# Optimization experiments

Measured on AMD Instinct MI355X. Metric: run time of the kernel, lower is better.

Reference implementation:

```python
import jax, jax.numpy as jnp
import numpy as np

N = 8192
E = 262144
IN_F = 128
OUT_F = 128


def setup_inputs() -> dict:
    key = jax.random.key(0)
    k1, k2, k3, k4 = jax.random.split(key, 4)
    x = jax.random.normal(k1, (N, IN_F), dtype=jnp.float32)
    adj = jax.random.randint(k2, (2, E), 0, N, dtype=jnp.int64)
    edge_w = jax.random.uniform(k3, (E,), dtype=jnp.float32)
    # Kaiming-normal-style init for weight (std = sqrt(2/fan_in)); zero bias.
    weight = jax.random.normal(k4, (IN_F, OUT_F), dtype=jnp.float32) * np.sqrt(2.0 / IN_F)
    bias = jnp.zeros((OUT_F,), dtype=jnp.float32)
    return {"x": x, "adj": adj, "edge_w": edge_w, "weight": weight, "bias": bias}


def reference(x, adj, edge_w, weight, bias):
    eps = 1e-10
    n = x.shape[0]
    support = x @ weight  # [N, out_features]
    # Densify COO adjacency (duplicate indices sum, matching sparse_coo_tensor.to_dense)
    adj_dense = jnp.zeros((n, n), dtype=x.dtype).at[adj[0], adj[1]].add(edge_w)
    adj_dense = adj_dense + jnp.eye(n, dtype=x.dtype)  # add self-loops
    deg = jnp.sum(adj_dense, axis=1)  # [N]
    d_inv_sqrt = 1.0 / jnp.sqrt(deg + eps)
    # D^{-1/2} A D^{-1/2} expressed as row/col scaling (same math as diag matmuls)
    norm_adj = d_inv_sqrt[:, None] * adj_dense * d_inv_sqrt[None, :]
    # include_bias=True path
    return norm_adj @ support + bias
```

## Files before the change

kernel.cpp:

```cpp
#include <hip/hip_runtime.h>
#include <math.h>

#define N_NODES 8192
#define NE      262144
#define F       128
#define CAP     96
#define NBLK    64
#define EPB     4096
#define GBLKS   256

#define FMA4(acc, xs, wq) \
    acc.x += (xs) * (wq).x; acc.y += (xs) * (wq).y; acc.z += (xs) * (wq).z; acc.w += (xs) * (wq).w;

__global__ __launch_bounds__(256) void k_fused(const float* __restrict__ x,
                                               const int* __restrict__ adj,
                                               const float* __restrict__ ew,
                                               const float* __restrict__ wmat,
                                               int* __restrict__ start_out,
                                               int2* __restrict__ bins,
                                               float* __restrict__ support) {
    __shared__ union {
        struct { int cnt[N_NODES]; int2 bin[EPB]; int part[256]; } e;
        struct { float xT[128][68]; float wl[128][68]; } g;
    } sh;
    int tid = threadIdx.x;

    if (blockIdx.x < NBLK) {
        int blk = blockIdx.x;
#pragma unroll
        for (int j = 0; j < 8; j++)
            *(int4*)&sh.e.cnt[tid * 4 + j * 1024] = make_int4(0, 0, 0, 0);
        __syncthreads();

        int base_e = blk * EPB + tid * 16;
        int4 r4[4];
#pragma unroll
        for (int ch = 0; ch < 4; ch++) r4[ch] = *(const int4*)(adj + base_e + ch * 4);
#pragma unroll
        for (int ch = 0; ch < 4; ch++) {
            atomicAdd(&sh.e.cnt[r4[ch].x], 1);
            atomicAdd(&sh.e.cnt[r4[ch].y], 1);
            atomicAdd(&sh.e.cnt[r4[ch].z], 1);
            atomicAdd(&sh.e.cnt[r4[ch].w], 1);
        }
        __syncthreads();

        int loc[32];
        int run = 0;
#pragma unroll
        for (int k = 0; k < 32; k++) { loc[k] = run; run += sh.e.cnt[tid * 32 + k]; }
        sh.e.part[tid] = run;
        __syncthreads();
        for (int off = 1; off < 256; off <<= 1) {
            int v = (tid >= off) ? sh.e.part[tid - off] : 0;
            __syncthreads();
            sh.e.part[tid] += v;
            __syncthreads();
        }
        int base0 = sh.e.part[tid] - run;
        __syncthreads();
#pragma unroll
        for (int k = 0; k < 32; k++) sh.e.cnt[tid * 32 + k] = base0 + loc[k];
        __syncthreads();
#pragma unroll
        for (int j = 0; j < 8; j++)
            *(int4*)&start_out[(size_t)blk * N_NODES + tid * 4 + j * 1024] =
                *(int4*)&sh.e.cnt[tid * 4 + j * 1024];
        __syncthreads();

#pragma unroll
        for (int ch = 0; ch < 4; ch++) {
            int e0 = base_e + ch * 4;
            int4   cc = *(const int4*)(adj + NE + e0);
            float4 wv = *(const float4*)(ew + e0);
            int pos;
            pos = atomicAdd(&sh.e.cnt[r4[ch].x], 1); sh.e.bin[pos] = make_int2(cc.x, __float_as_int(wv.x));
            pos = atomicAdd(&sh.e.cnt[r4[ch].y], 1); sh.e.bin[pos] = make_int2(cc.y, __float_as_int(wv.y));
            pos = atomicAdd(&sh.e.cnt[r4[ch].z], 1); sh.e.bin[pos] = make_int2(cc.z, __float_as_int(wv.z));
            pos = atomicAdd(&sh.e.cnt[r4[ch].w], 1); sh.e.bin[pos] = make_int2(cc.w, __float_as_int(wv.w));
        }
        __syncthreads();
#pragma unroll
        for (int j = 0; j < 8; j++)
            ((int4*)bins)[(size_t)blk * 2048 + tid + j * 256] =
                ((int4*)sh.e.bin)[tid + j * 256];
        return;
    }

    int g   = blockIdx.x - NBLK;
    int R0  = (g >> 1) * 64;
    int chf = g & 1;
    {
        int row = tid & 63;
        int w0  = tid >> 6;
        const float* xr = x + (size_t)(R0 + row) * F;
#pragma unroll
        for (int j = 0; j < 8; j++) {
            int c0 = w0 * 4 + 16 * j;
            float4 v = *(const float4*)(xr + c0);
            sh.g.xT[c0 + 0][row] = v.x;
            sh.g.xT[c0 + 1][row] = v.y;
            sh.g.xT[c0 + 2][row] = v.z;
            sh.g.xT[c0 + 3][row] = v.w;
        }
    }
    {
#pragma unroll
        for (int j = 0; j < 8; j++) {
            int q  = tid + 256 * j;
            int k  = q & 127;
            int c0 = 4 * (q >> 7);
            float4 v = *(const float4*)(wmat + (size_t)k * F + chf * 64 + c0);
            *(float4*)&sh.g.wl[k][c0] = v;
        }
    }
    __syncthreads();

    if (tid >= 128) return;

    int w  = tid >> 6;
    int l  = tid & 63;
    int r0 = (l >> 3) * 8;
    int c0 = w * 32 + (l & 7) * 4;

    float4 a0 = {0,0,0,0}, a1 = {0,0,0,0}, a2 = {0,0,0,0}, a3 = {0,0,0,0};
    float4 a4 = {0,0,0,0}, a5 = {0,0,0,0}, a6 = {0,0,0,0}, a7 = {0,0,0,0};
#pragma unroll 4
    for (int k = 0; k < F; k++) {
        float4 xv0 = *(const float4*)&sh.g.xT[k][r0];
        float4 xv1 = *(const float4*)&sh.g.xT[k][r0 + 4];
        float4 wq  = *(const float4*)&sh.g.wl[k][c0];
        FMA4(a0, xv0.x, wq); FMA4(a1, xv0.y, wq); FMA4(a2, xv0.z, wq); FMA4(a3, xv0.w, wq);
        FMA4(a4, xv1.x, wq); FMA4(a5, xv1.y, wq); FMA4(a6, xv1.z, wq); FMA4(a7, xv1.w, wq);
    }
    float* sp = support + (size_t)(R0 + r0) * F + chf * 64 + c0;
    *(float4*)(sp + 0 * F) = a0;  *(float4*)(sp + 1 * F) = a1;
    *(float4*)(sp + 2 * F) = a2;  *(float4*)(sp + 3 * F) = a3;
    *(float4*)(sp + 4 * F) = a4;  *(float4*)(sp + 5 * F) = a5;
    *(float4*)(sp + 6 * F) = a6;  *(float4*)(sp + 7 * F) = a7;
}

__global__ __launch_bounds__(256) void k_merge(const int* __restrict__ start_out,
                                               const int2* __restrict__ bins,
                                               int* __restrict__ cnt_dense,
                                               int2* __restrict__ dense,
                                               float* __restrict__ deg) {
    __shared__ int   starts_l[NBLK][32];
    __shared__ int   cnts[NBLK][32];
    __shared__ int   pref[NBLK][32];
    __shared__ float wsum[32];
    __shared__ int   tot[32];
    int tid = threadIdx.x;
    int r0  = blockIdx.x * 32;

    if (tid < 32) wsum[tid] = 0.f;
#pragma unroll
    for (int p = 0; p < 8; p++) {
        int blk = p * 8 + (tid >> 5);
        int row = tid & 31;
        int gr  = r0 + row;
        int s = start_out[(size_t)blk * N_NODES + gr];
        int e = (gr == N_NODES - 1) ? EPB : start_out[(size_t)blk * N_NODES + gr + 1];
        starts_l[blk][row] = s;
        cnts[blk][row] = e - s;
    }
    __syncthreads();
    if (tid < 32) {
        int run = 0;
#pragma unroll 8
        for (int k = 0; k < NBLK; k++) { pref[k][tid] = run; run += cnts[k][tid]; }
        tot[tid] = run;
    }
    __syncthreads();
#pragma unroll
    for (int j = 0; j < 8; j++) {
        int cell = j * 256 + tid;
        int blk  = cell >> 5;
        int row  = cell & 31;
        int n    = cnts[blk][row];
        if (n == 0) continue;
        int s    = starts_l[blk][row];
        int base = pref[blk][row];
        const int2* src = bins + (size_t)blk * EPB + s;
        int2* dst = dense + (size_t)(r0 + row) * CAP;
        float ws = 0.f;
        for (int k = 0; k < n; k++) {
            int2 e = src[k];
            ws += __int_as_float(e.y);
            if (base + k < CAP) dst[base + k] = e;
        }
        atomicAdd(&wsum[row], ws);
    }
    __syncthreads();
    if (tid < 32) {
        deg[r0 + tid] = wsum[tid];
        int t = tot[tid];
        cnt_dense[r0 + tid] = t < CAP ? t : CAP;
    }
}

__global__ __launch_bounds__(256) void k_spmm(const float* __restrict__ support,
                                              const float* __restrict__ deg,
                                              const int* __restrict__ cnt_dense,
                                              const int2* __restrict__ dense,
                                              const float* __restrict__ bias,
                                              float* __restrict__ out) {
    int l = threadIdx.x & 63;
    int i = blockIdx.x * 4 + (threadIdx.x >> 6);
    int f = l * 2;
    float2 bv = *(const float2*)(bias + f);
    float di = rsqrtf(deg[i] + 1.0f + 1e-10f);
    int cnt = cnt_dense[i];
    const int2* row = dense + (size_t)i * CAP;
    float2 a0 = *(const float2*)(support + (size_t)i * F + f);
    a0.x *= di; a0.y *= di;
    float2 a1 = {0.f, 0.f}, a2 = {0.f, 0.f}, a3 = {0.f, 0.f};
    int j = 0;
    for (; j + 4 <= cnt; j += 4) {
        int2 p0 = row[j + 0];
        int2 p1 = row[j + 1];
        int2 p2 = row[j + 2];
        int2 p3 = row[j + 3];
        float c0 = __int_as_float(p0.y) * rsqrtf(deg[p0.x] + 1.0f + 1e-10f);
        float c1 = __int_as_float(p1.y) * rsqrtf(deg[p1.x] + 1.0f + 1e-10f);
        float c2 = __int_as_float(p2.y) * rsqrtf(deg[p2.x] + 1.0f + 1e-10f);
        float c3 = __int_as_float(p3.y) * rsqrtf(deg[p3.x] + 1.0f + 1e-10f);
        float2 s0 = *(const float2*)(support + (size_t)p0.x * F + f);
        float2 s1 = *(const float2*)(support + (size_t)p1.x * F + f);
        float2 s2 = *(const float2*)(support + (size_t)p2.x * F + f);
        float2 s3 = *(const float2*)(support + (size_t)p3.x * F + f);
        a0.x += c0 * s0.x; a0.y += c0 * s0.y;
        a1.x += c1 * s1.x; a1.y += c1 * s1.y;
        a2.x += c2 * s2.x; a2.y += c2 * s2.y;
        a3.x += c3 * s3.x; a3.y += c3 * s3.y;
    }
    for (; j < cnt; j++) {
        int2 p = row[j];
        float cc = __int_as_float(p.y) * rsqrtf(deg[p.x] + 1.0f + 1e-10f);
        float2 sv = *(const float2*)(support + (size_t)p.x * F + f);
        a0.x += cc * sv.x; a0.y += cc * sv.y;
    }
    float2 r;
    r.x = di * ((a0.x + a1.x) + (a2.x + a3.x)) + bv.x;
    r.y = di * ((a0.y + a1.y) + (a2.y + a3.y)) + bv.y;
    *(float2*)(out + (size_t)i * F + f) = r;
}

extern "C" void kernel_launch(void* const* d_in, const int* in_sizes, int n_in,
                              void* d_out, int out_size, void* d_ws, size_t ws_size,
                              hipStream_t stream) {
    const float* x    = (const float*)d_in[0];
    const int*   adj  = (const int*)d_in[1];
    const float* ew   = (const float*)d_in[2];
    const float* w    = (const float*)d_in[3];
    const float* bias = (const float*)d_in[4];
    float* out = (float*)d_out;

    char*  ws        = (char*)d_ws;
    float* support   = (float*)(ws);
    float* deg       = (float*)(ws + (4u << 20));
    int*   cnt_dense = (int*)  (ws + (4u << 20) + 32768);
    int2*  dense     = (int2*) (ws + (4u << 20) + 65536);
    int*   start_out = (int*)  (ws + (11u << 20));
    int2*  bins      = (int2*) (ws + (13u << 20));

    k_fused<<<NBLK + GBLKS, 256, 0, stream>>>(x, adj, ew, w, start_out, bins, support);
    k_merge<<<N_NODES / 32, 256, 0, stream>>>(start_out, bins, cnt_dense, dense, deg);
    k_spmm<<<N_NODES / 4, 256, 0, stream>>>(support, deg, cnt_dense, dense, bias, out);
}
```

Measured before the change: 115.2 us.

## Double binning blocks and pad shared counter array to avoid bank conflicts

Splits the edge-binning phase across 128 blocks of 2048 edges instead of 64 blocks of 4096, giving more parallelism in the fused kernel's sort phase. It also pads the per-row shared counter array (one extra slot per 32 entries) so the per-thread serial scan over 32 consecutive counters avoids LDS bank conflicts. In exchange, the merge kernel now reads twice as many per-block start offsets and walks twice as many (smaller) segments per row, and the start_out buffer doubles, which moves the bins workspace offset.

After: 119.6 us. +3.8%, slower.

```diff
diff --git a/kernel.cpp b/kernel.cpp
--- a/kernel.cpp
+++ b/kernel.cpp
@@ -5,9 +5,12 @@
 #define NE      262144
 #define F       128
 #define CAP     96
-#define NBLK    64
-#define EPB     4096
+#define NBLK    128
+#define EPB     2048
 #define GBLKS   256
+
+#define A(row) ((row) + ((row) >> 5))
+#define CNT_SZ (N_NODES + N_NODES / 32)
 
 #define FMA4(acc, xs, wq) \
     acc.x += (xs) * (wq).x; acc.y += (xs) * (wq).y; acc.z += (xs) * (wq).z; acc.w += (xs) * (wq).w;
@@ -20,35 +23,35 @@
                                                int2* __restrict__ bins,
                                                float* __restrict__ support) {
     __shared__ union {
-        struct { int cnt[N_NODES]; int2 bin[EPB]; int part[256]; } e;
+        struct { int cnt[CNT_SZ]; int2 bin[EPB]; int part[256]; } e;
         struct { float xT[128][68]; float wl[128][68]; } g;
     } sh;
     int tid = threadIdx.x;
 
     if (blockIdx.x < NBLK) {
         int blk = blockIdx.x;
-#pragma unroll
-        for (int j = 0; j < 8; j++)
-            *(int4*)&sh.e.cnt[tid * 4 + j * 1024] = make_int4(0, 0, 0, 0);
-        __syncthreads();
-
-        int base_e = blk * EPB + tid * 16;
-        int4 r4[4];
-#pragma unroll
-        for (int ch = 0; ch < 4; ch++) r4[ch] = *(const int4*)(adj + base_e + ch * 4);
-#pragma unroll
-        for (int ch = 0; ch < 4; ch++) {
-            atomicAdd(&sh.e.cnt[r4[ch].x], 1);
-            atomicAdd(&sh.e.cnt[r4[ch].y], 1);
-            atomicAdd(&sh.e.cnt[r4[ch].z], 1);
-            atomicAdd(&sh.e.cnt[r4[ch].w], 1);
-        }
-        __syncthreads();
-
+        for (int j = tid; j < CNT_SZ / 4; j += 256)
+            ((int4*)sh.e.cnt)[j] = make_int4(0, 0, 0, 0);
+        __syncthreads();
+
+        int base_e = blk * EPB + tid * 8;
+        int4 r4[2];
+        r4[0] = *(const int4*)(adj + base_e);
+        r4[1] = *(const int4*)(adj + base_e + 4);
+#pragma unroll
+        for (int ch = 0; ch < 2; ch++) {
+            atomicAdd(&sh.e.cnt[A(r4[ch].x)], 1);
+            atomicAdd(&sh.e.cnt[A(r4[ch].y)], 1);
+            atomicAdd(&sh.e.cnt[A(r4[ch].z)], 1);
+            atomicAdd(&sh.e.cnt[A(r4[ch].w)], 1);
+        }
+        __syncthreads();
+
+        int base_l = 33 * tid;
         int loc[32];
         int run = 0;
 #pragma unroll
-        for (int k = 0; k < 32; k++) { loc[k] = run; run += sh.e.cnt[tid * 32 + k]; }
+        for (int k = 0; k < 32; k++) { loc[k] = run; run += sh.e.cnt[base_l + k]; }
         sh.e.part[tid] = run;
         __syncthreads();
         for (int off = 1; off < 256; off <<= 1) {
@@ -60,29 +63,32 @@
         int base0 = sh.e.part[tid] - run;
         __syncthreads();
 #pragma unroll
-        for (int k = 0; k < 32; k++) sh.e.cnt[tid * 32 + k] = base0 + loc[k];
-        __syncthreads();
-#pragma unroll
-        for (int j = 0; j < 8; j++)
-            *(int4*)&start_out[(size_t)blk * N_NODES + tid * 4 + j * 1024] =
-                *(int4*)&sh.e.cnt[tid * 4 + j * 1024];
-        __syncthreads();
-
-#pragma unroll
-        for (int ch = 0; ch < 4; ch++) {
+        for (int k = 0; k < 32; k++) sh.e.cnt[base_l + k] = base0 + loc[k];
+        __syncthreads();
+#pragma unroll
+        for (int j = 0; j < 8; j++) {
+            int row = tid * 4 + j * 1024;
+            int4 v = make_int4(sh.e.cnt[A(row)], sh.e.cnt[A(row + 1)],
+                               sh.e.cnt[A(row + 2)], sh.e.cnt[A(row + 3)]);
+            *(int4*)&start_out[(size_t)blk * N_NODES + row] = v;
+        }
+        __syncthreads();
+
+#pragma unroll
+        for (int ch = 0; ch < 2; ch++) {
             int e0 = base_e + ch * 4;
             int4   cc = *(const int4*)(adj + NE + e0);
             float4 wv = *(const float4*)(ew + e0);
             int pos;
-            pos = atomicAdd(&sh.e.cnt[r4[ch].x], 1); sh.e.bin[pos] = make_int2(cc.x, __float_as_int(wv.x));
-            pos = atomicAdd(&sh.e.cnt[r4[ch].y], 1); sh.e.bin[pos] = make_int2(cc.y, __float_as_int(wv.y));
-            pos = atomicAdd(&sh.e.cnt[r4[ch].z], 1); sh.e.bin[pos] = make_int2(cc.z, __float_as_int(wv.z));
-            pos = atomicAdd(&sh.e.cnt[r4[ch].w], 1); sh.e.bin[pos] = make_int2(cc.w, __float_as_int(wv.w));
-        }
-        __syncthreads();
-#pragma unroll
-        for (int j = 0; j < 8; j++)
-            ((int4*)bins)[(size_t)blk * 2048 + tid + j * 256] =
+            pos = atomicAdd(&sh.e.cnt[A(r4[ch].x)], 1); sh.e.bin[pos] = make_int2(cc.x, __float_as_int(wv.x));
+            pos = atomicAdd(&sh.e.cnt[A(r4[ch].y)], 1); sh.e.bin[pos] = make_int2(cc.y, __float_as_int(wv.y));
+            pos = atomicAdd(&sh.e.cnt[A(r4[ch].z)], 1); sh.e.bin[pos] = make_int2(cc.z, __float_as_int(wv.z));
+            pos = atomicAdd(&sh.e.cnt[A(r4[ch].w)], 1); sh.e.bin[pos] = make_int2(cc.w, __float_as_int(wv.w));
+        }
+        __syncthreads();
+#pragma unroll
+        for (int j = 0; j < 4; j++)
+            ((int4*)bins)[(size_t)blk * 1024 + tid + j * 256] =
                 ((int4*)sh.e.bin)[tid + j * 256];
         return;
     }
@@ -155,7 +161,7 @@
 
     if (tid < 32) wsum[tid] = 0.f;
 #pragma unroll
-    for (int p = 0; p < 8; p++) {
+    for (int p = 0; p < 16; p++) {
         int blk = p * 8 + (tid >> 5);
         int row = tid & 31;
         int gr  = r0 + row;
@@ -167,13 +173,12 @@
     __syncthreads();
     if (tid < 32) {
         int run = 0;
-#pragma unroll 8
         for (int k = 0; k < NBLK; k++) { pref[k][tid] = run; run += cnts[k][tid]; }
         tot[tid] = run;
     }
     __syncthreads();
 #pragma unroll
-    for (int j = 0; j < 8; j++) {
+    for (int j = 0; j < 16; j++) {
         int cell = j * 256 + tid;
         int blk  = cell >> 5;
         int row  = cell & 31;
@@ -262,7 +267,7 @@
     int*   cnt_dense = (int*)  (ws + (4u << 20) + 32768);
     int2*  dense     = (int2*) (ws + (4u << 20) + 65536);
     int*   start_out = (int*)  (ws + (11u << 20));
-    int2*  bins      = (int2*) (ws + (13u << 20));
+    int2*  bins      = (int2*) (ws + (16u << 20));
 
     k_fused<<<NBLK + GBLKS, 256, 0, stream>>>(x, adj, ew, w, start_out, bins, support);
     k_merge<<<N_NODES / 32, 256, 0, stream>>>(start_out, bins, cnt_dense, dense, deg);
```
